# Optimization experiments

Hardware: AMD Instinct MI355X
Metric: run time of the kernel (lower is better)

The kernel has to match this reference:

```python
import jax, jax.numpy as jnp
import numpy as np

B, N, K, F, E = 2, 16384, 32, 64, 16


def setup_inputs() -> dict:
    key = jax.random.key(0)
    k1, k2, k3, k4 = jax.random.split(key, 4)
    nodes = jax.random.normal(k1, (B, N, F), dtype=jnp.float32)
    # neighbor list: for each (batch, node) a list of K neighbor node indices
    nlist = jax.random.randint(k2, (B, N, K), 0, N, dtype=jnp.int32)
    edges = jax.random.normal(k3, (B, N, K, E), dtype=jnp.float32)
    # learned weight: (node_feat, node_feat, edge_feat) as in build()
    w = jax.random.normal(k4, (F, F, E), dtype=jnp.float32) * 0.05
    return {"nodes": nodes, "nlist": nlist, "edges": edges, "w": w}


def reference(nodes, nlist, edges, w):
    # tf.gather_nd(nodes, nlist): gather neighbor features -> [B, N, K, F]
    batch_idx = jnp.arange(nodes.shape[0], dtype=nlist.dtype)[:, None, None]
    sliced = nodes[batch_idx, nlist]  # [B, N, K, F]
    # edge-conditioned contraction: edges[b,i,j,n] * sliced[b,i,j,l] * w[l,m,n]
    prod = jnp.einsum('bijn,bijl,lmn->bijm', edges, sliced, w)  # [B, N, K, F]
    # mean over the K neighbors (axis=2); activation is None
    reduced = jnp.mean(prod, axis=2)  # [B, N, F]
    return reduced
```

## Files before the change

### kernel.cpp

```cpp
#include <hip/hip_runtime.h>
#include <cstdint>
#include <cstddef>

#define LOGN 14

typedef __bf16 bf16x8 __attribute__((ext_vector_type(8)));
typedef float f32x4 __attribute__((ext_vector_type(4)));
typedef unsigned u32;

#define BARRIER() __builtin_amdgcn_s_barrier()
#define LGKM0()   __builtin_amdgcn_s_waitcnt(0xC07F)

__device__ __forceinline__ u32 fbits(float f) { return __builtin_bit_cast(u32, f); }
__device__ __forceinline__ u32 pkrne(float lo, float hi) {
  u32 a = fbits(lo); a = a + 0x7fffu + ((a >> 16) & 1u);
  u32 b = fbits(hi); b = b + 0x7fffu + ((b >> 16) & 1u);
  return (b & 0xffff0000u) | (a >> 16);
}

__global__ void prep_wt(const float* __restrict__ w, unsigned short* __restrict__ wt) {
  int idx = blockIdx.x * 256 + threadIdx.x;
  int m = idx >> 10, k = idx & 1023, l = k >> 4, n = k & 15;
  u32 u = fbits(w[l * 1024 + m * 16 + n] * 0.03125f);
  wt[idx] = (unsigned short)((u + 0x7fffu + ((u >> 16) & 1u)) >> 16);
}

__device__ __forceinline__ bf16x8 mk_bw(const float* wp) {
  float v[8];
  #pragma unroll
  for (int i = 0; i < 8; ++i) v[i] = wp[i] * 0.03125f;
  uint4 pk{pkrne(v[0], v[1]), pkrne(v[2], v[3]), pkrne(v[4], v[5]), pkrne(v[6], v[7])};
  return __builtin_bit_cast(bf16x8, pk);
}

template <bool USE_WT>
__global__ __launch_bounds__(256, 3)
void mp_kernel(const float* __restrict__ nodes, const int* __restrict__ nlist,
               const float* __restrict__ edges, const unsigned short* __restrict__ wt,
               const float* __restrict__ w, float* __restrict__ out) {
  __shared__ u32 g_lds[16 * 512];
  __shared__ u32 sbuf[32 * 65];
  __shared__ u32 ebuf[32 * 22];

  const int tid = threadIdx.x;
  const int lane = tid & 63;
  const int wid = __builtin_amdgcn_readfirstlane(tid >> 6);
  const int q = lane >> 4, c = lane & 15;

  const int blk = blockIdx.x;
  const int xcd = blk & 7;
  const int batch = xcd >> 2;
  const int ordinal = ((blk >> 3) << 2) + (xcd & 3);
  const int wg0 = (batch << LOGN) + (ordinal << 4);
  const float* __restrict__ nbase = nodes + ((size_t)batch << 20);

  const int* __restrict__ nlp = nlist + (((size_t)wg0) << 5) + (wid << 3);
  const int2 nlv = *(const int2*)(nlp + ((lane >> 2) << 5) + ((lane & 3) << 1));

  float gv[2][8];
  float2 ge[2];

  const float* __restrict__ ebase = edges + (((size_t)wg0) << 9) + (wid << 7);

  #define ISSUE(p, slot)                                                        \
    {                                                                           \
      _Pragma("unroll")                                                         \
      for (int i = 0; i < 8; ++i) {                                             \
        const int ix = __builtin_amdgcn_readlane((i & 1) ? nlv.y : nlv.x,       \
                                                 4 * (p) + (i >> 1));           \
        gv[slot][i] = nbase[(((size_t)(u32)ix) << 6) + lane];                   \
      }                                                                         \
      ge[slot] = *(const float2*)(ebase + ((p) << 9) + (lane << 1));            \
    }

  ISSUE(0, 0)
  ISSUE(1, 1)

  const int erow = (wid << 3) + (lane >> 3);
  const int ecol = (lane & 7) << 1;

  #pragma unroll
  for (int p = 0; p < 16; ++p) {
    const int slot = p & 1;
    BARRIER();
    #pragma unroll
    for (int i = 0; i < 8; ++i)
      sbuf[((wid << 3) + i) * 65 + lane] = fbits(gv[slot][i]);
    *(uint2*)&ebuf[erow * 22 + ecol] = uint2{fbits(ge[slot].x), fbits(ge[slot].y)};
    if (p < 14) ISSUE(p + 2, slot)
    LGKM0();
    BARRIER();
    {
      const float* ef = (const float*)ebuf;
      const float* sf = (const float*)sbuf;
      float e[8];
      #pragma unroll
      for (int i = 0; i < 8; ++i) e[i] = ef[(q * 8 + i) * 22 + c];
      uint4 apk{pkrne(e[0], e[1]), pkrne(e[2], e[3]), pkrne(e[4], e[5]), pkrne(e[6], e[7])};
      float s[8];
      #pragma unroll
      for (int i = 0; i < 8; ++i) s[i] = sf[(q * 8 + i) * 65 + (wid << 4) + c];
      uint4 spk{pkrne(s[0], s[1]), pkrne(s[2], s[3]), pkrne(s[4], s[5]), pkrne(s[6], s[7])};
      f32x4 acc{0.f, 0.f, 0.f, 0.f};
      acc = __builtin_amdgcn_mfma_f32_16x16x32_bf16(__builtin_bit_cast(bf16x8, apk),
                                                    __builtin_bit_cast(bf16x8, spk),
                                                    acc, 0, 0, 0);
      const u32 lo = pkrne(acc[0], acc[1]);
      const u32 hi = pkrne(acc[2], acc[3]);
      const int chunk = (((wid << 4) + c) * 2 + (q >> 1)) ^ (p & 7);
      *(uint2*)&g_lds[(p << 9) + (chunk << 2) + ((q & 1) << 1)] = uint2{lo, hi};
    }
  }
  #undef ISSUE

  LGKM0();
  BARRIER();

  const int m = (wid << 4) + c;
  f32x4 ob{0.f, 0.f, 0.f, 0.f};
  if (USE_WT) {
    const unsigned short* wb = wt + ((size_t)m << 10) + (q << 3);
    #pragma unroll 8
    for (int s = 0; s < 32; ++s) {
      uint4 ar = *(const uint4*)&g_lds[(c << 9) + ((((s << 2) + q) ^ (c & 7)) << 2)];
      ob = __builtin_amdgcn_mfma_f32_16x16x32_bf16(__builtin_bit_cast(bf16x8, ar),
                                                   *(const bf16x8*)(wb + (s << 5)),
                                                   ob, 0, 0, 0);
    }
  } else {
    #pragma unroll 4
    for (int s = 0; s < 32; ++s) {
      uint4 ar = *(const uint4*)&g_lds[(c << 9) + ((((s << 2) + q) ^ (c & 7)) << 2)];
      const int l = 2 * s + (q >> 1);
      const float* wp = w + l * 1024 + m * 16 + ((q & 1) << 3);
      ob = __builtin_amdgcn_mfma_f32_16x16x32_bf16(__builtin_bit_cast(bf16x8, ar),
                                                   mk_bw(wp), ob, 0, 0, 0);
    }
  }

  #pragma unroll
  for (int r = 0; r < 4; ++r)
    out[((size_t)(wg0 + (q << 2) + r) << 6) + m] = ob[r];
}

extern "C" void kernel_launch(void* const* d_in, const int* in_sizes, int n_in,
                              void* d_out, int out_size, void* d_ws, size_t ws_size,
                              hipStream_t stream) {
  const float* nodes = (const float*)d_in[0];
  const int*   nlist = (const int*)d_in[1];
  const float* edges = (const float*)d_in[2];
  const float* w     = (const float*)d_in[3];
  float* out = (float*)d_out;

  if (ws_size >= 131072) {
    unsigned short* wt = (unsigned short*)d_ws;
    prep_wt<<<256, 256, 0, stream>>>(w, wt);
    mp_kernel<true><<<2048, 256, 0, stream>>>(nodes, nlist, edges, wt, w, out);
  } else {
    mp_kernel<false><<<2048, 256, 0, stream>>>(nodes, nlist, edges, nullptr, w, out);
  }
}
```

Before: 149.8 us.

## Give each wave whole nodes and load MFMA operands directly into registers

Each wave now owns four nodes. Per lane, it loads neighbor indices and then the gathered node features and edges straight into registers in the MFMA operand layout. This removes the sbuf/ebuf LDS staging and the per-step barriers. A two-deep software pipeline overlaps the index loads, gathers and MFMAs. The trade is many more scalar-strided global loads (4-byte accesses strided by 16 floats) plus higher register pressure from 80 floats of buffers.

New measurement: 148.1 us. Within noise of the previous version (-1.2%).

```diff
diff --git a/kernel.cpp b/kernel.cpp
--- a/kernel.cpp
+++ b/kernel.cpp
@@ -39,8 +39,6 @@
                const float* __restrict__ edges, const unsigned short* __restrict__ wt,
                const float* __restrict__ w, float* __restrict__ out) {
   __shared__ u32 g_lds[16 * 512];
-  __shared__ u32 sbuf[32 * 65];
-  __shared__ u32 ebuf[32 * 22];
 
   const int tid = threadIdx.x;
   const int lane = tid & 63;
@@ -54,64 +52,62 @@
   const int wg0 = (batch << LOGN) + (ordinal << 4);
   const float* __restrict__ nbase = nodes + ((size_t)batch << 20);
 
-  const int* __restrict__ nlp = nlist + (((size_t)wg0) << 5) + (wid << 3);
-  const int2 nlv = *(const int2*)(nlp + ((lane >> 2) << 5) + ((lane & 3) << 1));
+  const int nd0 = wid << 2;
 
-  float gv[2][8];
-  float2 ge[2];
-
-  const float* __restrict__ ebase = edges + (((size_t)wg0) << 9) + (wid << 7);
-
-  #define ISSUE(p, slot)                                                        \
-    {                                                                           \
-      _Pragma("unroll")                                                         \
-      for (int i = 0; i < 8; ++i) {                                             \
-        const int ix = __builtin_amdgcn_readlane((i & 1) ? nlv.y : nlv.x,       \
-                                                 4 * (p) + (i >> 1));           \
-        gv[slot][i] = nbase[(((size_t)(u32)ix) << 6) + lane];                   \
-      }                                                                         \
-      ge[slot] = *(const float2*)(ebase + ((p) << 9) + (lane << 1));            \
+  auto issue_nl = [&](int t, int4* ni) {
+    const int* r = nlist + (((size_t)(wg0 + nd0 + t)) << 5) + (q << 3);
+    ni[0] = *(const int4*)r;
+    ni[1] = *(const int4*)(r + 4);
+  };
+  auto issue_se = [&](int t, const int4* ni, float* S, float* E) {
+    const int ix[8] = {ni[0].x, ni[0].y, ni[0].z, ni[0].w,
+                       ni[1].x, ni[1].y, ni[1].z, ni[1].w};
+    #pragma unroll
+    for (int i = 0; i < 8; ++i) {
+      const float* rp = nbase + ((size_t)(u32)ix[i] << 6) + c;
+      #pragma unroll
+      for (int lt = 0; lt < 4; ++lt) S[i * 4 + lt] = rp[lt << 4];
     }
-
-  ISSUE(0, 0)
-  ISSUE(1, 1)
-
-  const int erow = (wid << 3) + (lane >> 3);
-  const int ecol = (lane & 7) << 1;
-
-  #pragma unroll
-  for (int p = 0; p < 16; ++p) {
-    const int slot = p & 1;
-    BARRIER();
+    const float* ep = edges + (((size_t)(wg0 + nd0 + t)) << 9) + (q << 7) + c;
     #pragma unroll
-    for (int i = 0; i < 8; ++i)
-      sbuf[((wid << 3) + i) * 65 + lane] = fbits(gv[slot][i]);
-    *(uint2*)&ebuf[erow * 22 + ecol] = uint2{fbits(ge[slot].x), fbits(ge[slot].y)};
-    if (p < 14) ISSUE(p + 2, slot)
-    LGKM0();
-    BARRIER();
-    {
-      const float* ef = (const float*)ebuf;
-      const float* sf = (const float*)sbuf;
-      float e[8];
-      #pragma unroll
-      for (int i = 0; i < 8; ++i) e[i] = ef[(q * 8 + i) * 22 + c];
-      uint4 apk{pkrne(e[0], e[1]), pkrne(e[2], e[3]), pkrne(e[4], e[5]), pkrne(e[6], e[7])};
-      float s[8];
-      #pragma unroll
-      for (int i = 0; i < 8; ++i) s[i] = sf[(q * 8 + i) * 65 + (wid << 4) + c];
-      uint4 spk{pkrne(s[0], s[1]), pkrne(s[2], s[3]), pkrne(s[4], s[5]), pkrne(s[6], s[7])};
+    for (int i = 0; i < 8; ++i) E[i] = ep[i << 4];
+  };
+  auto consume = [&](int p, const float* S, const float* E) {
+    uint4 apk{pkrne(E[0], E[1]), pkrne(E[2], E[3]),
+              pkrne(E[4], E[5]), pkrne(E[6], E[7])};
+    const bf16x8 af = __builtin_bit_cast(bf16x8, apk);
+    #pragma unroll
+    for (int lt = 0; lt < 4; ++lt) {
+      uint4 spk{pkrne(S[0 * 4 + lt], S[1 * 4 + lt]),
+                pkrne(S[2 * 4 + lt], S[3 * 4 + lt]),
+                pkrne(S[4 * 4 + lt], S[5 * 4 + lt]),
+                pkrne(S[6 * 4 + lt], S[7 * 4 + lt])};
       f32x4 acc{0.f, 0.f, 0.f, 0.f};
-      acc = __builtin_amdgcn_mfma_f32_16x16x32_bf16(__builtin_bit_cast(bf16x8, apk),
-                                                    __builtin_bit_cast(bf16x8, spk),
-                                                    acc, 0, 0, 0);
+      acc = __builtin_amdgcn_mfma_f32_16x16x32_bf16(af,
+              __builtin_bit_cast(bf16x8, spk), acc, 0, 0, 0);
       const u32 lo = pkrne(acc[0], acc[1]);
       const u32 hi = pkrne(acc[2], acc[3]);
-      const int chunk = (((wid << 4) + c) * 2 + (q >> 1)) ^ (p & 7);
+      const int chunk = ((((lt << 4) + c) << 1) + (q >> 1)) ^ (p & 7);
       *(uint2*)&g_lds[(p << 9) + (chunk << 2) + ((q & 1) << 1)] = uint2{lo, hi};
     }
+  };
+
+  {
+    int4 ni0[2], ni1[2];
+    float S0[32], E0[8], S1[32], E1[8];
+    issue_nl(0, ni0);
+    issue_nl(1, ni1);
+    issue_se(0, ni0, S0, E0);
+    issue_nl(2, ni0);
+    issue_se(1, ni1, S1, E1);
+    issue_nl(3, ni1);
+    consume(nd0 + 0, S0, E0);
+    issue_se(2, ni0, S0, E0);
+    consume(nd0 + 1, S1, E1);
+    issue_se(3, ni1, S1, E1);
+    consume(nd0 + 2, S0, E0);
+    consume(nd0 + 3, S1, E1);
   }
-  #undef ISSUE
 
   LGKM0();
   BARRIER();
```
